# Kernel tuning notes

Hardware: AMD Instinct MI355X
Metric: run time of the kernel (lower is better)

## Reference

```python
import jax, jax.numpy as jnp
import numpy as np

EMB = 1024
HEADS = 16
EPS = 1e-6


def setup_inputs() -> dict:
    key = jax.random.key(0)
    ks = jax.random.split(key, 11)
    B, T = 4, 2048
    s = 0.02
    inp = {
        "x": jax.random.normal(ks[0], (B, T, EMB), dtype=jnp.float32),
        "Wq": jax.random.normal(ks[1], (EMB, EMB), dtype=jnp.float32) * s,
        "bq": jnp.zeros((EMB,), dtype=jnp.float32),
        "Wk": jax.random.normal(ks[2], (EMB, EMB), dtype=jnp.float32) * s,
        "bk": jnp.zeros((EMB,), dtype=jnp.float32),
        "Wv": jax.random.normal(ks[3], (EMB, EMB), dtype=jnp.float32) * s,
        "bv": jnp.zeros((EMB,), dtype=jnp.float32),
        "Wp": jax.random.normal(ks[4], (EMB, EMB), dtype=jnp.float32) * s,
        "bp": jnp.zeros((EMB,), dtype=jnp.float32),
        "gamma": jnp.ones((EMB,), dtype=jnp.float32),
        "beta": jnp.zeros((EMB,), dtype=jnp.float32),
    }
    return inp


def reference(x, Wq, bq, Wk, bk, Wv, bv, Wp, bp, gamma, beta):
    B, T, E = x.shape
    H = HEADS
    hd = E // H
    residual = x
    # torch Linear: y = x @ W.T + b
    q = (jnp.einsum('bte,fe->btf', x, Wq) + bq).reshape(B, T, H, hd).transpose(0, 2, 1, 3)
    k = (jnp.einsum('bte,fe->btf', x, Wk) + bk).reshape(B, T, H, hd).transpose(0, 2, 1, 3)
    v = (jnp.einsum('bte,fe->btf', x, Wv) + bv).reshape(B, T, H, hd).transpose(0, 2, 1, 3)
    # NOTE: original scales by 1/sqrt(T), not 1/sqrt(head_size)
    scale = 1.0 / jnp.sqrt(jnp.asarray(T, dtype=x.dtype))
    att = jnp.einsum('bhqd,bhkd->bhqk', q, k) * scale
    causal = jnp.tril(jnp.ones((T, T), dtype=bool))
    att = jnp.where(causal, att, -jnp.inf)
    att = jax.nn.softmax(att, axis=-1)
    out = jnp.einsum('bhqk,bhkd->bhqd', att, v)
    out = out.transpose(0, 2, 1, 3).reshape(B, T, E)
    # residual added BEFORE projection (as in original)
    out = jnp.einsum('bte,fe->btf', out + residual, Wp) + bp
    # LayerNorm(eps=1e-6)
    mu = jnp.mean(out, axis=-1, keepdims=True)
    var = jnp.mean(jnp.square(out - mu), axis=-1, keepdims=True)
    out = (out - mu) / jnp.sqrt(var + EPS) * gamma + beta
    return out
```

## Files before the change

### kernel.cpp

```cpp
#include <hip/hip_runtime.h>
#include <hip/hip_bf16.h>
#include <cstdint>
#include <cstdio>

#define EMB    1024
#define HEADS  16
#define HD     64
#define TSEQ   2048
#define NBATCH 4
#define BT     (NBATCH*TSEQ)
#define QKVN   3072
#define QKLD   2048

#define CSCALE (1.4426950408889634f * 0.022097086912079608f)

typedef __hip_bfloat16 bf16;
typedef __attribute__((ext_vector_type(8))) short short8;
typedef __attribute__((ext_vector_type(4))) short short4v;
typedef __attribute__((ext_vector_type(4))) float f32x4;

#define MFMA32(A,B,C) __builtin_amdgcn_mfma_f32_16x16x32_bf16(A,B,C,0,0,0)
#if __has_builtin(__builtin_amdgcn_mfma_f32_16x16x16_bf16)
#define MFMA16(A,B,C) __builtin_amdgcn_mfma_f32_16x16x16_bf16(A,B,C,0,0,0)
#else
#define MFMA16(A,B,C) __builtin_amdgcn_mfma_f32_16x16x16bf16_1k(A,B,C,0,0,0)
#endif

#if __has_builtin(__builtin_amdgcn_exp2f)
#define EXP2(x) __builtin_amdgcn_exp2f(x)
#else
#define EXP2(x) exp2f(x)
#endif

template<bool B> struct BoolC { static constexpr bool value = B; };

__device__ __forceinline__ void gload_lds16(const void* g, void* l) {
  __builtin_amdgcn_global_load_lds(
      (const __attribute__((address_space(1))) void*)g,
      (__attribute__((address_space(3))) void*)l,
      16, 0, 0);
}

__device__ __forceinline__ unsigned pkbf(float a, float b) {
  unsigned ua = __builtin_bit_cast(unsigned, a) + 0x8000u;
  unsigned ub = __builtin_bit_cast(unsigned, b) + 0x8000u;
  return __builtin_amdgcn_perm(ub, ua, 0x07060302u);
}

#define BARRIER() do { asm volatile("" ::: "memory"); \
                       __builtin_amdgcn_s_barrier(); \
                       asm volatile("" ::: "memory"); } while (0)
#define BAR_VM(N) do { asm volatile("s_waitcnt vmcnt(" #N ")" ::: "memory"); \
                       __builtin_amdgcn_s_barrier(); \
                       asm volatile("" ::: "memory"); } while (0)

__global__ void fused_cast(const float* __restrict__ x, const float* __restrict__ Wq,
                           const float* __restrict__ Wk, const float* __restrict__ Wv,
                           const float* __restrict__ Wp, const float* __restrict__ bq,
                           const float* __restrict__ bk, const float* __restrict__ bv,
                           bf16* __restrict__ xb, bf16* __restrict__ wqkv,
                           bf16* __restrict__ wpb, float* __restrict__ biasqkv) {
  const int blk = blockIdx.x;
  const int i = threadIdx.x * 4;
  if (blk >= 12288) {
    const int wsel = blk - 12288;
    const float* bsrc = wsel == 0 ? bq : (wsel == 1 ? bk : bv);
    float4 bv4 = *(const float4*)(bsrc + i);
    if (wsel == 0) { bv4.x *= CSCALE; bv4.y *= CSCALE; bv4.z *= CSCALE; bv4.w *= CSCALE; }
    *(float4*)(biasqkv + wsel * 1024 + i) = bv4;
    return;
  }
  const float* src; bf16* dst; float sc = 1.0f;
  if (blk < 8192)       { src = x  + (size_t)blk * 1024;           dst = xb   + (size_t)blk * 1024; }
  else if (blk < 9216)  { src = Wq + (size_t)(blk - 8192) * 1024;  dst = wqkv + (size_t)(blk - 8192) * 1024; sc = CSCALE; }
  else if (blk < 10240) { src = Wk + (size_t)(blk - 9216) * 1024;  dst = wqkv + ((size_t)1 << 20) + (size_t)(blk - 9216) * 1024; }
  else if (blk < 11264) { src = Wv + (size_t)(blk - 10240) * 1024; dst = wqkv + ((size_t)2 << 20) + (size_t)(blk - 10240) * 1024; }
  else                  { src = Wp + (size_t)(blk - 11264) * 1024; dst = wpb  + (size_t)(blk - 11264) * 1024; }
  float4 v = *(const float4*)(src + i);
  union { short4v v; bf16 b[4]; } u;
  u.b[0] = __float2bfloat16(v.x * sc); u.b[1] = __float2bfloat16(v.y * sc);
  u.b[2] = __float2bfloat16(v.z * sc); u.b[3] = __float2bfloat16(v.w * sc);
  *(short4v*)(dst + i) = u.v;
}

#define PHASE_MFMA(MI0, NJ0) do { \
  __builtin_amdgcn_s_setprio(1); \
  _Pragma("unroll") \
  for (int m2 = 0; m2 < 4; ++m2) { \
    _Pragma("unroll") \
    for (int n2 = 0; n2 < 2; ++n2) { \
      acc[(MI0)+m2][(NJ0)+n2] = MFMA32(af[m2][0], bfr[(NJ0)+n2][0], acc[(MI0)+m2][(NJ0)+n2]); \
      acc[(MI0)+m2][(NJ0)+n2] = MFMA32(af[m2][1], bfr[(NJ0)+n2][1], acc[(MI0)+m2][(NJ0)+n2]); \
    } \
  } \
  __builtin_amdgcn_s_setprio(0); \
} while (0)

#define TILE(T, P) { \
  const int kn = ((T) + 1) * 64; \
  const bool st = (T) < 15; \
  const char* aB = rdA + (P) * 32768; \
  const char* bB = rdB + (P) * 32768; \
  char* sA = ldsA + ((P) ^ 1) * 32768 + wbase; \
  char* sB = ldsB + ((P) ^ 1) * 32768 + wbase; \
   \
  _Pragma("unroll") \
  for (int m2 = 0; m2 < 4; ++m2) { \
    af[m2][0] = *(const short8*)(aB + m2 * 2048 + cs0); \
    af[m2][1] = *(const short8*)(aB + m2 * 2048 + cs1); \
  } \
  _Pragma("unroll") \
  for (int n2 = 0; n2 < 2; ++n2) { \
    bfr[n2][0] = *(const short8*)(bB + n2 * 2048 + cs0); \
    bfr[n2][1] = *(const short8*)(bB + n2 * 2048 + cs1); \
  } \
  if (st) { gload_lds16(gB + kn,          sB);         \
            gload_lds16(gB + 131072 + kn, sB + 16384); } \
  BARRIER(); \
  PHASE_MFMA(0, 0); \
  BARRIER(); \
   \
  _Pragma("unroll") \
  for (int n2 = 2; n2 < 4; ++n2) { \
    bfr[n2][0] = *(const short8*)(bB + n2 * 2048 + cs0); \
    bfr[n2][1] = *(const short8*)(bB + n2 * 2048 + cs1); \
  } \
  if (st) { gload_lds16(gA + kn,          sA);         \
            gload_lds16(gA + 131072 + kn, sA + 16384); } \
  BARRIER(); \
  PHASE_MFMA(0, 2); \
  if (st) { BAR_VM(4); } else { BAR_VM(0); } \
   \
  _Pragma("unroll") \
  for (int m2 = 0; m2 < 4; ++m2) { \
    af[m2][0] = *(const short8*)(aB + (4 + m2) * 2048 + cs0); \
    af[m2][1] = *(const short8*)(aB + (4 + m2) * 2048 + cs1); \
  } \
  if (st) { gload_lds16(gB + 65536 + kn,  sB + 8192);  \
            gload_lds16(gB + 196608 + kn, sB + 24576); } \
  BARRIER(); \
  PHASE_MFMA(4, 2); \
  BARRIER(); \
   \
  if (st) { gload_lds16(gA + 65536 + kn,  sA + 8192);  \
            gload_lds16(gA + 196608 + kn, sA + 24576); } \
  PHASE_MFMA(4, 0); \
  if (st) { BAR_VM(2); } \
}

__global__ __launch_bounds__(512, 2) void gemm_qkv8(
    const bf16* __restrict__ A, const bf16* __restrict__ B,
    const float* __restrict__ bias, bf16* __restrict__ qkout,
    bf16* __restrict__ vt) {
  __shared__ short smem[65536];
  const int tid = threadIdx.x;
  const int l = tid & 63, w = tid >> 6;
  const int r = l & 15, qd = l >> 4;
  const int wm = w >> 2, wn = w & 3;

  const int f0 = blockIdx.x;
  const int sid = (f0 & 7) * 48 + (f0 >> 3);
  const int m0 = (sid / 12) * 256;
  const int n0 = (sid % 12) * 256;

  const int rowA = tid >> 3;
  const int chk = (tid & 7) ^ (rowA & 7);
  const bf16* gA = A + (size_t)(m0 + rowA) * 1024 + chk * 8;
  const bf16* gB = B + (size_t)(n0 + rowA) * 1024 + chk * 8;
  char* ldsA = (char*)smem;
  char* ldsB = (char*)smem + 65536;
  const int wbase = w * 1024;

  const char* rdA = (const char*)smem + wm * 16384 + r * 128;
  const char* rdB = (const char*)smem + 65536 + (wn >> 1) * 16384 +
                    ((wn & 1) * 64 + r) * 128;
  const int cs0 = (qd ^ (r & 7)) * 16;
  const int cs1 = ((4 + qd) ^ (r & 7)) * 16;

  f32x4 acc[8][4];
#pragma unroll
  for (int i = 0; i < 8; ++i)
#pragma unroll
    for (int j = 0; j < 4; ++j) acc[i][j] = (f32x4){0.f, 0.f, 0.f, 0.f};
  short8 af[4][2], bfr[4][2];

  {
    char* sA = ldsA + wbase;
    char* sB = ldsB + wbase;
    gload_lds16(gB,          sB);
    gload_lds16(gB + 131072, sB + 16384);
    gload_lds16(gA,          sA);
    gload_lds16(gA + 131072, sA + 16384);
    gload_lds16(gB + 65536,  sB + 8192);
    gload_lds16(gB + 196608, sB + 24576);
    gload_lds16(gA + 65536,  sA + 8192);
    gload_lds16(gA + 196608, sA + 24576);
    BAR_VM(2);
  }

#pragma unroll 1
  for (int tt = 0; tt < 8; ++tt) {
    TILE(tt * 2, 0)
    TILE(tt * 2 + 1, 1)
  }

  if (n0 < 2048) {
#pragma unroll
    for (int nt = 0; nt < 4; ++nt) {
      const int col = n0 + wn * 64 + nt * 16 + r;
      const float bv = bias[col];
#pragma unroll
      for (int mi = 0; mi < 8; ++mi) {
#pragma unroll
        for (int reg = 0; reg < 4; ++reg) {
          const int row = m0 + wm * 128 + mi * 16 + qd * 4 + reg;
          qkout[(size_t)row * QKLD + col] = __float2bfloat16(acc[mi][nt][reg] + bv);
        }
      }
    }
  } else {
    char* img = (char*)smem;
#pragma unroll
    for (int nt = 0; nt < 4; ++nt) {
      const int c_local = wn * 64 + nt * 16 + r;
      const float bv = bias[n0 + c_local];
      const int d7 = c_local & 7;
#pragma unroll
      for (int mi = 0; mi < 8; ++mi) {
        const int tbase = wm * 128 + mi * 16 + qd * 4;
        const int chunk = tbase >> 6;
        const int sbits = ((tbase >> 3) ^ d7) & 7;
        union { short4v v; bf16 b[4]; } u;
#pragma unroll
        for (int reg = 0; reg < 4; ++reg)
          u.b[reg] = __float2bfloat16(acc[mi][nt][reg] + bv);
        *(short4v*)(img + c_local * 512 + chunk * 128 + sbits * 16 + (qd & 1) * 8) = u.v;
      }
    }
    __syncthreads();
    const int bb = m0 >> 11, tb = m0 & 2047;
    const int hb = (n0 - 2048) >> 6;
    const int off = (tid & 31) * 16;
#pragma unroll
    for (int i = 0; i < 16; ++i) {
      const int row = i * 16 + (tid >> 5);
      const int h2 = hb + (row >> 6), d = row & 63;
      const f32x4 vv = *(const f32x4*)(img + row * 512 + off);
      char* dst = (char*)(vt + ((size_t)(bb * 16 + h2) * 64 + d) * 2048 + tb) + off;
      *(f32x4*)dst = vv;
    }
  }
}

#define PJ_MFMA(MI0) do { \
  __builtin_amdgcn_s_setprio(1); \
  _Pragma("unroll") \
  for (int m2 = 0; m2 < 2; ++m2) { \
    _Pragma("unroll") \
    for (int nj = 0; nj < 2; ++nj) { \
      acc[(MI0)+m2][nj] = MFMA32(af[m2][0], bfr[nj][0], acc[(MI0)+m2][nj]); \
      acc[(MI0)+m2][nj] = MFMA32(af[m2][1], bfr[nj][1], acc[(MI0)+m2][nj]); \
    } \
  } \
  __builtin_amdgcn_s_setprio(0); \
} while (0)

#define PJ_TILE(T, P) { \
  const int kn = ((T) + 1) * 64; \
  const bool st = (T) < 15; \
  const char* aB = rdA + (P) * 32768; \
  const char* bB = rdB + (P) * 16384; \
  char* sA = ldsA + ((P) ^ 1) * 32768 + wbase; \
  char* sB = ldsB + ((P) ^ 1) * 16384 + wbase; \
   \
  _Pragma("unroll") \
  for (int m2 = 0; m2 < 2; ++m2) { \
    af[m2][0] = *(const short8*)(aB + m2 * 2048 + cs0); \
    af[m2][1] = *(const short8*)(aB + m2 * 2048 + cs1); \
  } \
  _Pragma("unroll") \
  for (int nj = 0; nj < 2; ++nj) { \
    bfr[nj][0] = *(const short8*)(bB + nj * 2048 + cs0); \
    bfr[nj][1] = *(const short8*)(bB + nj * 2048 + cs1); \
  } \
  if (st) { gload_lds16(gB + kn,         sB); \
            gload_lds16(gB + 65536 + kn, sB + 8192); } \
  BARRIER(); \
  PJ_MFMA(0); \
  BARRIER(); \
   \
  _Pragma("unroll") \
  for (int m2 = 0; m2 < 2; ++m2) { \
    af[m2][0] = *(const short8*)(aB + (2 + m2) * 2048 + cs0); \
    af[m2][1] = *(const short8*)(aB + (2 + m2) * 2048 + cs1); \
  } \
  if (st) { gload_lds16(gA + kn,          sA); \
            gload_lds16(gA + 131072 + kn, sA + 16384); } \
  BARRIER(); \
  PJ_MFMA(2); \
  if (st) { BAR_VM(4); } else { BAR_VM(0); } \
   \
  _Pragma("unroll") \
  for (int m2 = 0; m2 < 2; ++m2) { \
    af[m2][0] = *(const short8*)(aB + (4 + m2) * 2048 + cs0); \
    af[m2][1] = *(const short8*)(aB + (4 + m2) * 2048 + cs1); \
  } \
  if (st) { gload_lds16(gA + 65536 + kn,  sA + 8192); \
            gload_lds16(gA + 196608 + kn, sA + 24576); } \
  BARRIER(); \
  PJ_MFMA(4); \
  BARRIER(); \
   \
  _Pragma("unroll") \
  for (int m2 = 0; m2 < 2; ++m2) { \
    af[m2][0] = *(const short8*)(aB + (6 + m2) * 2048 + cs0); \
    af[m2][1] = *(const short8*)(aB + (6 + m2) * 2048 + cs1); \
  } \
  PJ_MFMA(6); \
  if (st) { BAR_VM(2); } \
}

__global__ __launch_bounds__(512, 2) void gemm_proj8(
    const bf16* __restrict__ A, const bf16* __restrict__ B,
    const float* __restrict__ bias, float* __restrict__ out) {
  __shared__ short smem[49152];
  const int tid = threadIdx.x;
  const int l = tid & 63, w = tid >> 6;
  const int r = l & 15, qd = l >> 4;
  const int wm = w >> 2, wn = w & 3;

  const int f0 = blockIdx.x;
  const int sid = (f0 & 7) * 32 + (f0 >> 3);
  const int m0 = (sid >> 3) * 256;
  const int n0 = (sid & 7) * 128;

  const int rowA = tid >> 3;
  const int chk = (tid & 7) ^ (rowA & 7);
  const bf16* gA = A + (size_t)(m0 + rowA) * 1024 + chk * 8;
  const bf16* gB = B + (size_t)(n0 + rowA) * 1024 + chk * 8;
  char* ldsA = (char*)smem;
  char* ldsB = (char*)smem + 65536;
  const int wbase = w * 1024;

  const char* rdA = (const char*)smem + wm * 16384 + r * 128;
  const char* rdB = (const char*)smem + 65536 + (wn * 32 + r) * 128;
  const int cs0 = (qd ^ (r & 7)) * 16;
  const int cs1 = ((4 + qd) ^ (r & 7)) * 16;

  f32x4 acc[8][2];
#pragma unroll
  for (int i = 0; i < 8; ++i)
#pragma unroll
    for (int j = 0; j < 2; ++j) acc[i][j] = (f32x4){0.f, 0.f, 0.f, 0.f};
  short8 af[2][2], bfr[2][2];

  {
    char* sA = ldsA + wbase;
    char* sB = ldsB + wbase;
    gload_lds16(gB,          sB);
    gload_lds16(gB + 65536,  sB + 8192);
    gload_lds16(gA,          sA);
    gload_lds16(gA + 131072, sA + 16384);
    gload_lds16(gA + 65536,  sA + 8192);
    gload_lds16(gA + 196608, sA + 24576);
    BAR_VM(2);
  }

#pragma unroll 1
  for (int tt = 0; tt < 8; ++tt) {
    PJ_TILE(tt * 2, 0)
    PJ_TILE(tt * 2 + 1, 1)
  }

#pragma unroll
  for (int nj = 0; nj < 2; ++nj) {
    const int col = n0 + wn * 32 + nj * 16 + r;
    const float bv = bias[col];
#pragma unroll
    for (int mi = 0; mi < 8; ++mi) {
#pragma unroll
      for (int reg = 0; reg < 4; ++reg) {
        const int row = m0 + wm * 128 + mi * 16 + qd * 4 + reg;
        out[(size_t)row * 1024 + col] = acc[mi][nj][reg] + bv;
      }
    }
  }
}

__global__ __launch_bounds__(512, 2) void flash8(
    const bf16* __restrict__ qk, const bf16* __restrict__ vt,
    const float* __restrict__ x, bf16* __restrict__ pb) {
  const int bh = blockIdx.x;
  const int ip = blockIdx.y;
  const int b = bh >> 4, h = bh & 15;
  const int qt[4] = { 31 - ip, 23 - ip, ip + 8, ip };
  const int tid = threadIdx.x, l = tid & 63, w = tid >> 6;
  const int wg = w & 3, grp = w >> 2;
  const int r = l & 15, quad = l >> 4;

  __shared__ __align__(16) char smem[40960];

  const bf16* Qbase = qk + (size_t)b * TSEQ * QKLD + h * HD;
  const bf16* Kbase = Qbase + 1024;
  const bf16* Vhead = vt + (size_t)bh * 64 * 2048;

  const bf16* vg = Vhead + (size_t)(tid >> 3) * 2048 + (tid & 7) * 8;
  char* vdst = smem + w * 1024;

  short8 qf0[4], qf1[4];
#pragma unroll
  for (int t = 0; t < 4; ++t) {
    const bf16* qp = Qbase + (size_t)(qt[t] * 64 + wg * 16 + r) * QKLD + quad * 8;
    qf0[t] = *(const short8*)qp;
    qf1[t] = *(const short8*)(qp + 32);
  }

  f32x4 o[4][4], lac[4];
#pragma unroll
  for (int t = 0; t < 4; ++t) {
    lac[t] = (f32x4){0.f, 0.f, 0.f, 0.f};
#pragma unroll
    for (int nt = 0; nt < 4; ++nt) o[t][nt] = (f32x4){0.f, 0.f, 0.f, 0.f};
  }

  short4v ones4;
#pragma unroll
  for (int j = 0; j < 4; ++j) ones4[j] = (short)0x3F80;

  short4v vf[4][4];

  const bf16* Kl = Kbase + (size_t)r * QKLD + quad * 8;
  const int ktmax = qt[0];
  const int qrow_l = wg * 16 + r;

  gload_lds16(vg, vdst);
  gload_lds16(vg + 64, vdst + 8192);

  auto tilestep = [&](int t, auto diagc, short8 (&k0)[4], short8 (&k1)[4]) {
    constexpr bool D = decltype(diagc)::value;
    f32x4 s[4];
    __builtin_amdgcn_s_setprio(1);
#pragma unroll
    for (int g = 0; g < 4; ++g) {
      f32x4 a = (f32x4){0.f, 0.f, 0.f, 0.f};
      a = MFMA32(k0[g], qf0[t], a);
      a = MFMA32(k1[g], qf1[t], a);
      s[g] = a;
    }
    __builtin_amdgcn_s_setprio(0);
    short4v pA[4];
#pragma unroll
    for (int g = 0; g < 4; ++g) {
      float p[4];
#pragma unroll
      for (int reg = 0; reg < 4; ++reg) {
        float e = EXP2(s[g][reg]);
        if (D) {
          const int kj = g * 16 + quad * 4 + reg;
          if (kj > qrow_l) e = 0.f;
        }
        p[reg] = e;
      }
      union { short4v v; unsigned u[2]; } pu;
      pu.u[0] = pkbf(p[0], p[1]);
      pu.u[1] = pkbf(p[2], p[3]);
      pA[g] = pu.v;
    }
    __builtin_amdgcn_s_setprio(1);
#pragma unroll
    for (int nt = 0; nt < 4; ++nt)
#pragma unroll
      for (int g = 0; g < 4; ++g)
        o[t][nt] = MFMA16(pA[g], vf[nt][g], o[t][nt]);
#pragma unroll
    for (int g = 0; g < 4; ++g)
      lac[t] = MFMA16(pA[g], ones4, lac[t]);
    __builtin_amdgcn_s_setprio(0);
  };

  const int niter = (ktmax >> 1) + 1;
#pragma unroll 1
  for (int i = 0; i < niter; ++i) {
    const int kt = 2 * i + grp;
    const bool act = kt <= ktmax;
    short8 k0[4], k1[4];
    if (act) {
#pragma unroll
      for (int g = 0; g < 4; ++g) {
        const bf16* kp = Kl + (size_t)(kt * 64 + g * 16) * QKLD;
        k0[g] = *(const short8*)kp;
        k1[g] = *(const short8*)(kp + 32);
      }
    }
    __syncthreads();
    if (2 * i + 2 <= ktmax)
      gload_lds16(vg + (2 * i + 2) * 64, smem + ((2 * i + 2) & 3) * 8192 + w * 1024);
    if (2 * i + 3 <= ktmax)
      gload_lds16(vg + (2 * i + 3) * 64, smem + ((2 * i + 3) & 3) * 8192 + w * 1024);
    if (act) {
      const bf16* V = (const bf16*)smem + (kt & 3) * 4096;
#pragma unroll
      for (int nt = 0; nt < 4; ++nt)
#pragma unroll
        for (int g = 0; g < 4; ++g)
          vf[nt][g] = *(const short4v*)(V + (nt * 16 + r) * 64 +
                                        (((g * 2 + (quad >> 1)) ^ (r & 7)) * 8) + (quad & 1) * 4);
      if (kt == qt[0]) tilestep(0, BoolC<true>{}, k0, k1);
      else             tilestep(0, BoolC<false>{}, k0, k1);
      if (kt <= qt[1]) { if (kt == qt[1]) tilestep(1, BoolC<true>{}, k0, k1);
                         else             tilestep(1, BoolC<false>{}, k0, k1); }
      if (kt <= qt[2]) { if (kt == qt[2]) tilestep(2, BoolC<true>{}, k0, k1);
                         else             tilestep(2, BoolC<false>{}, k0, k1); }
      if (kt <= qt[3]) { if (kt == qt[3]) tilestep(3, BoolC<true>{}, k0, k1);
                         else             tilestep(3, BoolC<false>{}, k0, k1); }
    }
  }

  float* combO = (float*)smem;
  float* combL = (float*)(smem + 32768);
  const int lb128 = (wg * 64 + l) * 32;
  const int lbl = (wg * 64 + l) * 8;

  __syncthreads();
#pragma unroll
  for (int rnd = 0; rnd < 2; ++rnd) {
    const int wgrp = (rnd == 0) ? 1 : 0;
    if (grp == wgrp) {
#pragma unroll
      for (int t2 = 0; t2 < 2; ++t2) {
        const int tt = rnd * 2 + t2;
#pragma unroll
        for (int nt = 0; nt < 4; ++nt)
          *(f32x4*)&combO[lb128 + (((t2 * 4 + nt) ^ (l & 7)) << 2)] = o[tt][nt];
        *(f32x4*)&combL[lbl + t2 * 4] = lac[tt];
      }
    }
    __syncthreads();
    if (grp != wgrp) {
#pragma unroll
      for (int t2 = 0; t2 < 2; ++t2) {
        const int tt = rnd * 2 + t2;
        const f32x4 ls = *(const f32x4*)&combL[lbl + t2 * 4];
#pragma unroll
        for (int j2 = 0; j2 < 4; ++j2) lac[tt][j2] += ls[j2];
#pragma unroll
        for (int nt = 0; nt < 4; ++nt) {
          const f32x4 ov = *(const f32x4*)&combO[lb128 + (((t2 * 4 + nt) ^ (l & 7)) << 2)];
#pragma unroll
          for (int j2 = 0; j2 < 4; ++j2) o[tt][nt][j2] += ov[j2];
        }
#pragma unroll
        for (int reg = 0; reg < 4; ++reg) {
          const float inv = 1.0f / lac[tt][reg];
          const int row = qt[tt] * 64 + wg * 16 + quad * 4 + reg;
          const float* xr = x + (size_t)(b * TSEQ + row) * EMB + h * HD;
          bf16* pr = pb + (size_t)(b * TSEQ + row) * EMB + h * HD;
#pragma unroll
          for (int nt = 0; nt < 4; ++nt) {
            const int d = nt * 16 + r;
            pr[d] = __float2bfloat16(o[tt][nt][reg] * inv + xr[d]);
          }
        }
      }
    }
    if (rnd == 0) __syncthreads();
  }
}

__global__ __launch_bounds__(256) void ln_kernel(float* __restrict__ out,
                                                 const float* __restrict__ gamma,
                                                 const float* __restrict__ beta) {
  const int row = blockIdx.x;
  const int tid = threadIdx.x;
  float* p = out + (size_t)row * EMB;
  float4 v = ((const float4*)p)[tid];
  float s = v.x + v.y + v.z + v.w;
  float ss = v.x * v.x + v.y * v.y + v.z * v.z + v.w * v.w;
#pragma unroll
  for (int m = 1; m < 64; m <<= 1) {
    s += __shfl_xor(s, m, 64);
    ss += __shfl_xor(ss, m, 64);
  }
  __shared__ float red[8];
  const int w = tid >> 6, l = tid & 63;
  if (l == 0) { red[w] = s; red[4 + w] = ss; }
  __syncthreads();
  s = red[0] + red[1] + red[2] + red[3];
  ss = red[4] + red[5] + red[6] + red[7];
  const float mu = s * (1.0f / EMB);
  const float var = ss * (1.0f / EMB) - mu * mu;
  const float rs = rsqrtf(var + 1e-6f);
  const float4 g = ((const float4*)gamma)[tid];
  const float4 bb = ((const float4*)beta)[tid];
  float4 o;
  o.x = (v.x - mu) * rs * g.x + bb.x;
  o.y = (v.y - mu) * rs * g.y + bb.y;
  o.z = (v.z - mu) * rs * g.z + bb.z;
  o.w = (v.w - mu) * rs * g.w + bb.w;
  ((float4*)p)[tid] = o;
}

extern "C" void kernel_launch(void* const* d_in, const int* in_sizes, int n_in,
                              void* d_out, int out_size, void* d_ws, size_t ws_size,
                              hipStream_t stream) {
  const float* x     = (const float*)d_in[0];
  const float* Wq    = (const float*)d_in[1];
  const float* bq    = (const float*)d_in[2];
  const float* Wk    = (const float*)d_in[3];
  const float* bk    = (const float*)d_in[4];
  const float* Wv    = (const float*)d_in[5];
  const float* bv    = (const float*)d_in[6];
  const float* Wp    = (const float*)d_in[7];
  const float* bp    = (const float*)d_in[8];
  const float* gamma = (const float*)d_in[9];
  const float* beta  = (const float*)d_in[10];
  float* out = (float*)d_out;

  if (ws_size < (size_t)74 * 1024 * 1024) {
    printf("kernel_launch: ws_size %zu too small\n", ws_size);
    return;
  }
  char* ws = (char*)d_ws;
  bf16* xb    = (bf16*)ws;
  bf16* wqkv  = (bf16*)(ws + ((size_t)16 << 20));
  bf16* wpb   = (bf16*)(ws + ((size_t)22 << 20));
  float* bqkv = (float*)(ws + ((size_t)24 << 20));
  bf16* qkbuf = (bf16*)(ws + ((size_t)25 << 20));
  bf16* vtbuf = (bf16*)(ws + ((size_t)57 << 20));
  bf16* pbuf  = xb;

  fused_cast<<<12291, 256, 0, stream>>>(x, Wq, Wk, Wv, Wp, bq, bk, bv, xb, wqkv, wpb, bqkv);

  gemm_qkv8<<<dim3(384), dim3(512), 0, stream>>>(xb, wqkv, bqkv, qkbuf, vtbuf);

  flash8<<<dim3(64, 8), 512, 0, stream>>>(qkbuf, vtbuf, x, pbuf);

  gemm_proj8<<<dim3(256), dim3(512), 0, stream>>>(pbuf, wpb, bp, out);

  ln_kernel<<<BT, 256, 0, stream>>>(out, gamma, beta);
}
```

Measured before the change: 304.0 us.

## Stage K tiles through swizzled LDS ring alongside V in flash kernel

The flash attention kernel now brings K tiles into shared memory with asynchronous global-to-LDS loads, using an XOR swizzle and the same four-slot ring as V, instead of each wave reading K straight from global memory into registers. Shared memory grows to 64KB and the launch bound is raised to 4 blocks per CU. The aim is to overlap K fetches with compute and drop the redundant per-wave global reads of K. In exchange it adds LDS traffic and footprint, which may limit how many blocks can be resident.

```diff
diff --git a/kernel.cpp b/kernel.cpp
--- a/kernel.cpp
+++ b/kernel.cpp
@@ -387,7 +387,7 @@
   }
 }
 
-__global__ __launch_bounds__(512, 2) void flash8(
+__global__ __launch_bounds__(512, 4) void flash9(
     const bf16* __restrict__ qk, const bf16* __restrict__ vt,
     const float* __restrict__ x, bf16* __restrict__ pb) {
   const int bh = blockIdx.x;
@@ -398,14 +398,17 @@
   const int wg = w & 3, grp = w >> 2;
   const int r = l & 15, quad = l >> 4;
 
-  __shared__ __align__(16) char smem[40960];
+  __shared__ __align__(16) char smem[65536];
 
   const bf16* Qbase = qk + (size_t)b * TSEQ * QKLD + h * HD;
   const bf16* Kbase = Qbase + 1024;
   const bf16* Vhead = vt + (size_t)bh * 64 * 2048;
 
   const bf16* vg = Vhead + (size_t)(tid >> 3) * 2048 + (tid & 7) * 8;
-  char* vdst = smem + w * 1024;
+  const int krow = tid >> 3;
+  const bf16* kg = Kbase + (size_t)krow * QKLD + ((tid & 7) ^ (krow & 7)) * 8;
+  char* vbase = smem + w * 1024;
+  char* kbase = smem + 32768 + w * 1024;
 
   short8 qf0[4], qf1[4];
 #pragma unroll
@@ -429,12 +432,13 @@
 
   short4v vf[4][4];
 
-  const bf16* Kl = Kbase + (size_t)r * QKLD + quad * 8;
   const int ktmax = qt[0];
   const int qrow_l = wg * 16 + r;
 
-  gload_lds16(vg, vdst);
-  gload_lds16(vg + 64, vdst + 8192);
+  gload_lds16(vg,           vbase);
+  gload_lds16(vg + 64,      vbase + 8192);
+  gload_lds16(kg,           kbase);
+  gload_lds16(kg + 131072,  kbase + 8192);
 
   auto tilestep = [&](int t, auto diagc, short8 (&k0)[4], short8 (&k1)[4]) {
     constexpr bool D = decltype(diagc)::value;
@@ -483,28 +487,36 @@
   for (int i = 0; i < niter; ++i) {
     const int kt = 2 * i + grp;
     const bool act = kt <= ktmax;
-    short8 k0[4], k1[4];
+    __syncthreads();
+    const int nx0 = 2 * i + 2, nx1 = 2 * i + 3;
+    if (nx0 <= ktmax) {
+      gload_lds16(vg + nx0 * 64,            smem + (nx0 & 3) * 8192 + w * 1024);
+      gload_lds16(kg + (size_t)nx0 * 131072, smem + 32768 + (nx0 & 3) * 8192 + w * 1024);
+    }
+    if (nx1 <= ktmax) {
+      gload_lds16(vg + nx1 * 64,            smem + (nx1 & 3) * 8192 + w * 1024);
+      gload_lds16(kg + (size_t)nx1 * 131072, smem + 32768 + (nx1 & 3) * 8192 + w * 1024);
+    }
     if (act) {
-#pragma unroll
-      for (int g = 0; g < 4; ++g) {
-        const bf16* kp = Kl + (size_t)(kt * 64 + g * 16) * QKLD;
-        k0[g] = *(const short8*)kp;
-        k1[g] = *(const short8*)(kp + 32);
-      }
-    }
-    __syncthreads();
-    if (2 * i + 2 <= ktmax)
-      gload_lds16(vg + (2 * i + 2) * 64, smem + ((2 * i + 2) & 3) * 8192 + w * 1024);
-    if (2 * i + 3 <= ktmax)
-      gload_lds16(vg + (2 * i + 3) * 64, smem + ((2 * i + 3) & 3) * 8192 + w * 1024);
-    if (act) {
-      const bf16* V = (const bf16*)smem + (kt & 3) * 4096;
-#pragma unroll
-      for (int nt = 0; nt < 4; ++nt)
-#pragma unroll
-        for (int g = 0; g < 4; ++g)
-          vf[nt][g] = *(const short4v*)(V + (nt * 16 + r) * 64 +
-                                        (((g * 2 + (quad >> 1)) ^ (r & 7)) * 8) + (quad & 1) * 4);
+      short8 k0[4], k1[4];
+      {
+        const bf16* Kt = (const bf16*)(smem + 32768 + (kt & 3) * 8192);
+#pragma unroll
+        for (int g = 0; g < 4; ++g) {
+          const bf16* kp = Kt + (g * 16 + r) * 64;
+          k0[g] = *(const short8*)(kp + ((quad ^ (r & 7)) * 8));
+          k1[g] = *(const short8*)(kp + (((quad + 4) ^ (r & 7)) * 8));
+        }
+      }
+      {
+        const bf16* V = (const bf16*)smem + (kt & 3) * 4096;
+#pragma unroll
+        for (int nt = 0; nt < 4; ++nt)
+#pragma unroll
+          for (int g = 0; g < 4; ++g)
+            vf[nt][g] = *(const short4v*)(V + (nt * 16 + r) * 64 +
+                                          (((g * 2 + (quad >> 1)) ^ (r & 7)) * 8) + (quad & 1) * 4);
+      }
       if (kt == qt[0]) tilestep(0, BoolC<true>{}, k0, k1);
       else             tilestep(0, BoolC<false>{}, k0, k1);
       if (kt <= qt[1]) { if (kt == qt[1]) tilestep(1, BoolC<true>{}, k0, k1);
@@ -633,7 +645,7 @@
 
   gemm_qkv8<<<dim3(384), dim3(512), 0, stream>>>(xb, wqkv, bqkv, qkbuf, vtbuf);
 
-  flash8<<<dim3(64, 8), 512, 0, stream>>>(qkbuf, vtbuf, x, pbuf);
+  flash9<<<dim3(64, 8), 512, 0, stream>>>(qkbuf, vtbuf, x, pbuf);
 
   gemm_proj8<<<dim3(256), dim3(512), 0, stream>>>(pbuf, wpb, bp, out);
 
```

Measured after the change: 400.4 us. 1.32x slower.
